# Kernel tuning notes

Measured on AMD Instinct MI355X. Metric: run time of the kernel, lower is better.

## Reference

```python
import jax, jax.numpy as jnp
import numpy as np

D_MODEL = 1024
NHEAD = 16
DFF = 4096
MAXD = 32


def _ln(x, g, b, eps=1e-5):
    mu = jnp.mean(x, axis=-1, keepdims=True)
    var = jnp.mean(jnp.square(x - mu), axis=-1, keepdims=True)
    return (x - mu) * jax.lax.rsqrt(var + eps) * g + b


def setup_inputs() -> dict:
    key = jax.random.key(0)
    ks = jax.random.split(key, 16)
    D, F, H = D_MODEL, DFF, NHEAD
    s = 1.0 / np.sqrt(D)
    inp = {
        "src": jax.random.normal(ks[0], (2, 2048, D), dtype=jnp.float32),
        "Wq": jax.random.normal(ks[1], (D, D), dtype=jnp.float32) * s,
        "Wk": jax.random.normal(ks[2], (D, D), dtype=jnp.float32) * s,
        "Wv": jax.random.normal(ks[3], (D, D), dtype=jnp.float32) * s,
        "bq": jnp.zeros((D,), jnp.float32),
        "bk": jnp.zeros((D,), jnp.float32),
        "bv": jnp.zeros((D,), jnp.float32),
        "Wo": jax.random.normal(ks[4], (D, D), dtype=jnp.float32) * s,
        "bo": jnp.zeros((D,), jnp.float32),
        "rpe_table": jax.random.normal(ks[5], (2 * MAXD + 1, H), dtype=jnp.float32) * 0.02,
        "W1": jax.random.normal(ks[6], (D, F), dtype=jnp.float32) * s,
        "b1": jnp.zeros((F,), jnp.float32),
        "W2": jax.random.normal(ks[7], (F, D), dtype=jnp.float32) * (1.0 / np.sqrt(F)),
        "b2": jnp.zeros((D,), jnp.float32),
        "ln1_g": jnp.ones((D,), jnp.float32),
        "ln1_b": jnp.zeros((D,), jnp.float32),
        "ln2_g": jnp.ones((D,), jnp.float32),
        "ln2_b": jnp.zeros((D,), jnp.float32),
    }
    return inp


def reference(src, Wq, Wk, Wv, bq, bk, bv, Wo, bo, rpe_table, W1, b1, W2, b2,
              ln1_g, ln1_b, ln2_g, ln2_b):
    B, L, D = src.shape
    H = NHEAD
    Dh = D // H
    scale = 1.0 / jnp.sqrt(jnp.asarray(Dh, src.dtype))

    # relative position bias: [L, L, H] -> [H, L, L]
    pos = jnp.arange(L)
    rel = jnp.clip(pos[None, :] - pos[:, None], -MAXD, MAXD) + MAXD  # [L, L]
    bias = jnp.transpose(rpe_table[rel], (2, 0, 1))  # [H, L, L]

    q = (src @ Wq + bq).reshape(B, L, H, Dh)
    k = (src @ Wk + bk).reshape(B, L, H, Dh)
    v = (src @ Wv + bv).reshape(B, L, H, Dh)

    scores = jnp.einsum("blhd,bmhd->bhlm", q, k) * scale + bias[None]
    attn = jax.nn.softmax(scores, axis=-1)
    ctx = jnp.einsum("bhlm,bmhd->blhd", attn, v).reshape(B, L, D)
    attn_out = ctx @ Wo + bo

    x = _ln(src + attn_out, ln1_g, ln1_b)
    ff = jax.nn.relu(x @ W1 + b1) @ W2 + b2
    return _ln(x + ff, ln2_g, ln2_b)
```

## Files before the change

kernel.cpp:

```cpp
#include <hip/hip_runtime.h>
#include <hip/hip_bf16.h>

#define D_MODEL 1024
#define NHEAD 16
#define DH 64
#define DFF 4096
#define MAXD 32
#define L_ 2048
#define NROW 4096

typedef __attribute__((ext_vector_type(4))) float floatx4;
typedef __attribute__((ext_vector_type(8))) __bf16 bf16x8;
typedef __attribute__((ext_vector_type(4))) unsigned short ushort4v;

static __device__ inline unsigned short f2bf(float f) {
    __hip_bfloat16 h = __float2bfloat16(f);
    return __builtin_bit_cast(unsigned short, h);
}

static __device__ inline floatx4 mfma16(bf16x8 a, bf16x8 b, floatx4 c) {
    return __builtin_amdgcn_mfma_f32_16x16x32_bf16(a, b, c, 0, 0, 0);
}

static __device__ inline void gload_lds16(const unsigned short* g, unsigned short* l) {
    __builtin_amdgcn_global_load_lds((const __attribute__((address_space(1))) unsigned int*)g,
                                     (__attribute__((address_space(3))) unsigned int*)l,
                                     16, 0, 0);
}

__global__ __launch_bounds__(256) void cast_bf16_kernel(const float* __restrict__ in,
                                                        unsigned short* __restrict__ out, int n4) {
    int i = blockIdx.x * 256 + threadIdx.x;
    if (i < n4) {
        floatx4 v = *(const floatx4*)&in[(size_t)i * 4];
        ushort4v o;
        o.x = f2bf(v[0]); o.y = f2bf(v[1]); o.z = f2bf(v[2]); o.w = f2bf(v[3]);
        *(ushort4v*)&out[(size_t)i * 4] = o;
    }
}

__global__ __launch_bounds__(256) void transpose_cast_kernel(const float* __restrict__ W,
                                                             unsigned short* __restrict__ WT,
                                                             int K, int N) {
    __shared__ float tile[32][33];
    int k0 = blockIdx.y * 32, n0 = blockIdx.x * 32;
    for (int i = threadIdx.x; i < 1024; i += 256) {
        int r = i >> 5, c = i & 31;
        tile[r][c] = W[(size_t)(k0 + r) * N + n0 + c];
    }
    __syncthreads();
    for (int i = threadIdx.x; i < 1024; i += 256) {
        int r = i >> 5, c = i & 31;
        WT[(size_t)(n0 + r) * K + k0 + c] = f2bf(tile[c][r]);
    }
}

__global__ __launch_bounds__(256) void pack_bias_kernel(const float* __restrict__ bq,
                                                        const float* __restrict__ bk,
                                                        const float* __restrict__ bv,
                                                        float* __restrict__ out) {
    int i = blockIdx.x * 256 + threadIdx.x;
    if (i < 3072) out[i] = (i < 1024) ? bq[i] : ((i < 2048) ? bk[i - 1024] : bv[i - 2048]);
}

template <int NF, bool OUTBF16, bool RELU>
__global__ __launch_bounds__(256) void gemm_kernel(const unsigned short* __restrict__ A,
                                                   const unsigned short* __restrict__ BT,
                                                   const float* __restrict__ bias,
                                                   void* __restrict__ Cout,
                                                   int M, int N, int K) {
    constexpr int BN = NF * 32;
    __shared__ unsigned short Asm[128][32];
    __shared__ unsigned short Bsm[BN][32];
    int t = threadIdx.x;
    int lane = t & 63, w = t >> 6;
    int wm = w >> 1, wn = w & 1;
    int lr = lane & 15, hg = lane >> 4;
    int m0 = blockIdx.y * 128, n0 = blockIdx.x * BN;

    floatx4 acc[4][NF];
#pragma unroll
    for (int i = 0; i < 4; i++)
#pragma unroll
        for (int j = 0; j < NF; j++) acc[i][j] = (floatx4)0.0f;

    int r0 = t >> 2, c0 = (t & 3) * 8;

    for (int k0 = 0; k0 < K; k0 += 32) {
        __syncthreads();
        gload_lds16(&A[(size_t)(m0 + r0) * K + k0 + c0], &Asm[r0][c0]);
        gload_lds16(&A[(size_t)(m0 + r0 + 64) * K + k0 + c0], &Asm[r0 + 64][c0]);
        gload_lds16(&BT[(size_t)(n0 + r0) * K + k0 + c0], &Bsm[r0][c0]);
        if (NF == 4)
            gload_lds16(&BT[(size_t)(n0 + r0 + 64) * K + k0 + c0], &Bsm[r0 + 64][c0]);
        __syncthreads();
        bf16x8 af[4], bfg[NF];
#pragma unroll
        for (int mf = 0; mf < 4; mf++) af[mf] = *(const bf16x8*)&Asm[wm * 64 + mf * 16 + lr][hg * 8];
#pragma unroll
        for (int nf = 0; nf < NF; nf++)
            bfg[nf] = *(const bf16x8*)&Bsm[wn * NF * 16 + nf * 16 + lr][hg * 8];
#pragma unroll
        for (int mf = 0; mf < 4; mf++)
#pragma unroll
            for (int nf = 0; nf < NF; nf++) acc[mf][nf] = mfma16(af[mf], bfg[nf], acc[mf][nf]);
    }

#pragma unroll
    for (int mf = 0; mf < 4; mf++)
#pragma unroll
        for (int nf = 0; nf < NF; nf++) {
            int col = n0 + wn * NF * 16 + nf * 16 + lr;
            float bv = bias[col];
#pragma unroll
            for (int r = 0; r < 4; r++) {
                int row = m0 + wm * 64 + mf * 16 + hg * 4 + r;
                float v = acc[mf][nf][r] + bv;
                if (RELU) v = v > 0.f ? v : 0.f;
                if (OUTBF16)
                    ((unsigned short*)Cout)[(size_t)row * N + col] = f2bf(v);
                else
                    ((float*)Cout)[(size_t)row * N + col] = v;
            }
        }
}

__global__ __launch_bounds__(512, 4) void attn_kernel(const unsigned short* __restrict__ qkv,
                                                      const float* __restrict__ rpe,
                                                      unsigned short* __restrict__ ctx) {
    __shared__ unsigned short Kb0[64 * 64];
    __shared__ unsigned short Kb1[64 * 64];
    __shared__ unsigned short Vt[64 * 64];
    __shared__ unsigned short Ps[8][16 * 64];
    __shared__ float rpl[65];

    const int t = threadIdx.x;
    const int lane = t & 63, w = t >> 6;
    const int lr = lane & 15, hg = lane >> 4;
    const int lrs = (lr & 7) ^ (lr >> 3);

    const int blk = blockIdx.x;
    const int qb = blk & 15;
    const int h = (blk >> 4) & 15;
    const int b = blk >> 8;
    const int q0 = qb * 128;
    const int hcol = h * 64;
    const size_t rowbase = (size_t)b * L_ * 3072;

    const int kr = t >> 3, kch = t & 7;
    const int kswz = (kch ^ (kr & 7) ^ (kr >> 3)) & 7;
    unsigned short* kdst0 = &Kb0[kr * 64 + kch * 8];
    unsigned short* kdst1 = &Kb1[kr * 64 + kch * 8];

    if (t < 65) rpl[t] = rpe[t * NHEAD + h];

    const int qi = q0 + w * 16 + lr;
    bf16x8 qf0 = *(const bf16x8*)&qkv[rowbase + (size_t)qi * 3072 + hcol + hg * 8];
    bf16x8 qf1 = *(const bf16x8*)&qkv[rowbase + (size_t)qi * 3072 + hcol + 32 + hg * 8];

    gload_lds16(&qkv[rowbase + (size_t)kr * 3072 + 1024 + hcol + kswz * 8], kdst0);
    __syncthreads();

    float rpl0 = rpl[0], rpl64 = rpl[64];
    floatx4 o[4];
#pragma unroll
    for (int df = 0; df < 4; df++) o[df] = (floatx4)0.f;
    float mst = -1e30f, lst = 0.f;
    const float scale = 0.125f;
    unsigned short* PsW = &Ps[w][0];

#define ATT_STEP(KT, KcP, KnP, MORE)                                                               \
    {                                                                                              \
        const int key0 = (KT) * 64;                                                                \
        int4 tv = *(const int4*)&qkv[rowbase + (size_t)(key0 + kr) * 3072 + 2048 + hcol + kch * 8];\
        if (MORE)                                                                                  \
            gload_lds16(&qkv[rowbase + (size_t)(key0 + 64 + kr) * 3072 + 1024 + hcol + kswz * 8],  \
                        KnP);                                                                      \
        floatx4 st[4];                                                                             \
        _Pragma("unroll")                                                                          \
        for (int kf = 0; kf < 4; kf++) {                                                           \
            int sw = lrs ^ (kf * 2);                                                               \
            bf16x8 a0 = *(const bf16x8*)&(KcP)[(kf * 16 + lr) * 64 + ((hg ^ sw) << 3)];            \
            bf16x8 a1 = *(const bf16x8*)&(KcP)[(kf * 16 + lr) * 64 + (((4 + hg) ^ sw) << 3)];      \
            st[kf] = mfma16(a1, qf1, mfma16(a0, qf0, (floatx4)0.f));                               \
        }                                                                                          \
        bool rightC = (key0 > q0 + 159);                                                           \
        bool leftC = (key0 + 95 < q0);                                                             \
        float cbv = rightC ? rpl64 : rpl0;                                                         \
        float sv[16];                                                                              \
        float mx = -1e30f;                                                                         \
        if (leftC || rightC) {                                                                     \
            _Pragma("unroll")                                                                      \
            for (int kf = 0; kf < 4; kf++)                                                         \
                _Pragma("unroll")                                                                  \
                for (int r = 0; r < 4; r++) {                                                      \
                    float v = st[kf][r] * scale + cbv;                                             \
                    sv[kf * 4 + r] = v;                                                            \
                    mx = fmaxf(mx, v);                                                             \
                }                                                                                  \
        } else {                                                                                   \
            _Pragma("unroll")                                                                      \
            for (int kf = 0; kf < 4; kf++)                                                         \
                _Pragma("unroll")                                                                  \
                for (int r = 0; r < 4; r++) {                                                      \
                    int rel = key0 + kf * 16 + hg * 4 + r - qi;                                    \
                    rel = rel < -MAXD ? -MAXD : (rel > MAXD ? MAXD : rel);                         \
                    float v = st[kf][r] * scale + rpl[rel + MAXD];                                 \
                    sv[kf * 4 + r] = v;                                                            \
                    mx = fmaxf(mx, v);                                                             \
                }                                                                                  \
        }                                                                                          \
        mx = fmaxf(mx, __shfl_xor(mx, 16, 64));                                                    \
        mx = fmaxf(mx, __shfl_xor(mx, 32, 64));                                                    \
        float newm = fmaxf(mst, mx);                                                               \
        float corr = __expf(mst - newm);                                                           \
        mst = newm;                                                                                \
        float ps = 0.f;                                                                            \
        unsigned int pk[8];                                                                        \
        _Pragma("unroll")                                                                          \
        for (int kf = 0; kf < 4; kf++)                                                             \
            _Pragma("unroll")                                                                      \
            for (int j = 0; j < 2; j++) {                                                          \
                float p0 = __expf(sv[kf * 4 + 2 * j] - newm);                                      \
                float p1 = __expf(sv[kf * 4 + 2 * j + 1] - newm);                                  \
                ps += p0 + p1;                                                                     \
                pk[kf * 2 + j] = (unsigned int)f2bf(p0) | ((unsigned int)f2bf(p1) << 16);          \
            }                                                                                      \
        lst = lst * corr + ps;                                                                     \
        _Pragma("unroll")                                                                          \
        for (int df = 0; df < 4; df++) o[df] *= corr;                                              \
        _Pragma("unroll")                                                                          \
        for (int kf = 0; kf < 4; kf++)                                                             \
            _Pragma("unroll")                                                                      \
            for (int j = 0; j < 2; j++) {                                                          \
                int ch = ((kf * 2 + (hg >> 1)) ^ lrs) & 7;                                         \
                *(unsigned int*)&PsW[lr * 64 + (ch << 3) + (hg & 1) * 4 + 2 * j] = pk[kf * 2 + j]; \
            }                                                                                      \
        _Pragma("unroll")                                                                          \
        for (int e = 0; e < 8; e++) {                                                              \
            int d = kch * 8 + e;                                                                   \
            int ch = ((kr >> 3) ^ e ^ kch) & 7;                                                    \
            unsigned short val = (unsigned short)(((const unsigned int*)&tv)[e >> 1] >>            \
                                                  ((e & 1) * 16));                                 \
            Vt[d * 64 + (ch << 3) + (kr & 7)] = val;                                               \
        }                                                                                          \
        __syncthreads();                                                                           \
        bf16x8 pb0 = *(const bf16x8*)&PsW[lr * 64 + ((hg ^ lrs) << 3)];                            \
        bf16x8 pb1 = *(const bf16x8*)&PsW[lr * 64 + (((4 + hg) ^ lrs) << 3)];                      \
        _Pragma("unroll")                                                                          \
        for (int df = 0; df < 4; df++) {                                                           \
            int sw = lrs ^ (df * 2);                                                               \
            bf16x8 v0 = *(const bf16x8*)&Vt[(df * 16 + lr) * 64 + ((hg ^ sw) << 3)];               \
            bf16x8 v1 = *(const bf16x8*)&Vt[(df * 16 + lr) * 64 + (((4 + hg) ^ sw) << 3)];         \
            o[df] = mfma16(v1, pb1, mfma16(v0, pb0, o[df]));                                       \
        }                                                                                          \
        __syncthreads();                                                                           \
    }

    for (int kt = 0; kt < L_ / 64; kt += 2) {
        ATT_STEP(kt, Kb0, kdst1, true);
        ATT_STEP(kt + 1, Kb1, kdst0, (kt + 2 < L_ / 64));
    }
#undef ATT_STEP

    float rs = lst;
    rs += __shfl_xor(rs, 16, 64);
    rs += __shfl_xor(rs, 32, 64);
    float inv = 1.f / rs;
    size_t obase = (size_t)(b * L_ + qi) * 1024 + hcol;
#pragma unroll
    for (int df = 0; df < 4; df++)
#pragma unroll
        for (int r = 0; r < 4; r++)
            ctx[obase + df * 16 + hg * 4 + r] = f2bf(o[df][r] * inv);
}

template <bool WBF>
__global__ __launch_bounds__(256) void resln_kernel(const float* __restrict__ ra,
                                                    const float* __restrict__ rb,
                                                    const float* __restrict__ g,
                                                    const float* __restrict__ be,
                                                    float* __restrict__ outf,
                                                    unsigned short* __restrict__ outb) {
    __shared__ float red[4];
    __shared__ float red2[4];
    int row = blockIdx.x;
    int t = threadIdx.x;
    int w = t >> 6, lane = t & 63;
    size_t base = (size_t)row * 1024 + t * 4;
    floatx4 a = *(const floatx4*)&ra[base];
    floatx4 b = *(const floatx4*)&rb[base];
    floatx4 y = a + b;
    float s = y[0] + y[1] + y[2] + y[3];
#pragma unroll
    for (int d = 1; d < 64; d <<= 1) s += __shfl_xor(s, d, 64);
    if (lane == 0) red[w] = s;
    __syncthreads();
    float mu = (red[0] + red[1] + red[2] + red[3]) * (1.f / 1024.f);
    floatx4 d4 = y - mu;
    float sq = d4[0] * d4[0] + d4[1] * d4[1] + d4[2] * d4[2] + d4[3] * d4[3];
#pragma unroll
    for (int d = 1; d < 64; d <<= 1) sq += __shfl_xor(sq, d, 64);
    if (lane == 0) red2[w] = sq;
    __syncthreads();
    float var = (red2[0] + red2[1] + red2[2] + red2[3]) * (1.f / 1024.f);
    float rstd = rsqrtf(var + 1e-5f);
    floatx4 gg = *(const floatx4*)&g[t * 4];
    floatx4 bb = *(const floatx4*)&be[t * 4];
    floatx4 outv;
#pragma unroll
    for (int i = 0; i < 4; i++) outv[i] = d4[i] * rstd * gg[i] + bb[i];
    *(floatx4*)&outf[base] = outv;
    if (WBF) {
        ushort4v ov;
        ov.x = f2bf(outv[0]); ov.y = f2bf(outv[1]); ov.z = f2bf(outv[2]); ov.w = f2bf(outv[3]);
        *(ushort4v*)&outb[base] = ov;
    }
}

extern "C" void kernel_launch(void* const* d_in, const int* in_sizes, int n_in,
                              void* d_out, int out_size, void* d_ws, size_t ws_size,
                              hipStream_t stream) {
    const float* src = (const float*)d_in[0];
    const float* Wq = (const float*)d_in[1];
    const float* Wk = (const float*)d_in[2];
    const float* Wv = (const float*)d_in[3];
    const float* bq = (const float*)d_in[4];
    const float* bk = (const float*)d_in[5];
    const float* bv = (const float*)d_in[6];
    const float* Wo = (const float*)d_in[7];
    const float* bo = (const float*)d_in[8];
    const float* rpe = (const float*)d_in[9];
    const float* W1 = (const float*)d_in[10];
    const float* b1 = (const float*)d_in[11];
    const float* W2 = (const float*)d_in[12];
    const float* b2 = (const float*)d_in[13];
    const float* ln1g = (const float*)d_in[14];
    const float* ln1b = (const float*)d_in[15];
    const float* ln2g = (const float*)d_in[16];
    const float* ln2b = (const float*)d_in[17];
    float* out = (float*)d_out;
    char* ws = (char*)d_ws;

    const size_t o_srcb = 0;
    const size_t o_wtqkv = o_srcb + 8388608;
    const size_t o_wto = o_wtqkv + 6291456;
    const size_t o_wt1 = o_wto + 2097152;
    const size_t o_wt2 = o_wt1 + 8388608;
    const size_t o_bqkv = o_wt2 + 8388608;
    const size_t o_qkv = o_bqkv + 12288;
    const size_t o_ctxb = o_qkv + 25165824;
    const size_t o_x = o_ctxb + 8388608;
    const size_t o_hb = o_x + 16777216;

    unsigned short* srcb = (unsigned short*)(ws + o_srcb);
    unsigned short* wtqkv = (unsigned short*)(ws + o_wtqkv);
    unsigned short* wto = (unsigned short*)(ws + o_wto);
    unsigned short* wt1 = (unsigned short*)(ws + o_wt1);
    unsigned short* wt2 = (unsigned short*)(ws + o_wt2);
    float* bqkv = (float*)(ws + o_bqkv);
    unsigned short* qkvb = (unsigned short*)(ws + o_qkv);
    unsigned short* ctxb = (unsigned short*)(ws + o_ctxb);
    float* x = (float*)(ws + o_x);
    unsigned short* hb = (unsigned short*)(ws + o_hb);
    float* attnout = (float*)(ws + o_qkv);
    float* ff = (float*)(ws + o_qkv);
    unsigned short* xb = (unsigned short*)(ws + o_srcb);

    cast_bf16_kernel<<<4096, 256, 0, stream>>>(src, srcb, 1048576);
    transpose_cast_kernel<<<dim3(32, 32), 256, 0, stream>>>(Wq, wtqkv, 1024, 1024);
    transpose_cast_kernel<<<dim3(32, 32), 256, 0, stream>>>(Wk, wtqkv + 1024 * 1024, 1024, 1024);
    transpose_cast_kernel<<<dim3(32, 32), 256, 0, stream>>>(Wv, wtqkv + 2 * 1024 * 1024, 1024, 1024);
    transpose_cast_kernel<<<dim3(32, 32), 256, 0, stream>>>(Wo, wto, 1024, 1024);
    transpose_cast_kernel<<<dim3(128, 32), 256, 0, stream>>>(W1, wt1, 1024, 4096);
    transpose_cast_kernel<<<dim3(32, 128), 256, 0, stream>>>(W2, wt2, 4096, 1024);
    pack_bias_kernel<<<12, 256, 0, stream>>>(bq, bk, bv, bqkv);

    gemm_kernel<4, true, false><<<dim3(24, 32), 256, 0, stream>>>(srcb, wtqkv, bqkv, qkvb, NROW, 3072, 1024);
    attn_kernel<<<512, 512, 0, stream>>>(qkvb, rpe, ctxb);
    gemm_kernel<2, false, false><<<dim3(16, 32), 256, 0, stream>>>(ctxb, wto, bo, attnout, NROW, 1024, 1024);
    resln_kernel<true><<<4096, 256, 0, stream>>>(src, attnout, ln1g, ln1b, x, xb);
    gemm_kernel<4, true, true><<<dim3(32, 32), 256, 0, stream>>>(xb, wt1, b1, hb, NROW, 4096, 1024);
    gemm_kernel<2, false, false><<<dim3(16, 32), 256, 0, stream>>>(hb, wt2, b2, ff, NROW, 1024, 4096);
    resln_kernel<false><<<4096, 256, 0, stream>>>(x, ff, ln2g, ln2b, out, nullptr);
}
```

Measured before the change: 346.3 us.

## Double-buffer GEMM LDS tiles and shrink attention blocks to 64 queries

The GEMM kernel now uses two LDS buffers for A and B. It issues the next K-slice's async loads before computing on the current one, which overlaps global-to-LDS transfer with MFMA work and halves the number of barriers per K element. Separately, the attention kernel moves from 512-thread blocks covering 128 queries to 256-thread blocks covering 64 queries. Each thread now loads two K/V rows, and a block-index remap interleaves blocks across the grid. The attention change doubles the block count for better occupancy and load spread, but it doubles K/V reloads per query and increases LDS use in the GEMM.

```diff
diff --git a/kernel.cpp b/kernel.cpp
--- a/kernel.cpp
+++ b/kernel.cpp
@@ -63,6 +63,22 @@
     if (i < 3072) out[i] = (i < 1024) ? bq[i] : ((i < 2048) ? bk[i - 1024] : bv[i - 2048]);
 }
 
+#define GEMM_COMPUTE(As, Bs)                                                        \
+    {                                                                               \
+        bf16x8 af[4], bfg[NF];                                                      \
+        _Pragma("unroll")                                                           \
+        for (int mf = 0; mf < 4; mf++)                                              \
+            af[mf] = *(const bf16x8*)&As[wm * 64 + mf * 16 + lr][hg * 8];           \
+        _Pragma("unroll")                                                           \
+        for (int nf = 0; nf < NF; nf++)                                             \
+            bfg[nf] = *(const bf16x8*)&Bs[wn * NF * 16 + nf * 16 + lr][hg * 8];     \
+        _Pragma("unroll")                                                           \
+        for (int mf = 0; mf < 4; mf++)                                              \
+            _Pragma("unroll")                                                       \
+            for (int nf = 0; nf < NF; nf++)                                         \
+                acc[mf][nf] = mfma16(af[mf], bfg[nf], acc[mf][nf]);                 \
+    }
+
 template <int NF, bool OUTBF16, bool RELU>
 __global__ __launch_bounds__(256) void gemm_kernel(const unsigned short* __restrict__ A,
                                                    const unsigned short* __restrict__ BT,
@@ -70,8 +86,8 @@
                                                    void* __restrict__ Cout,
                                                    int M, int N, int K) {
     constexpr int BN = NF * 32;
-    __shared__ unsigned short Asm[128][32];
-    __shared__ unsigned short Bsm[BN][32];
+    __shared__ unsigned short A0[128][32], A1[128][32];
+    __shared__ unsigned short B0[BN][32], B1[BN][32];
     int t = threadIdx.x;
     int lane = t & 63, w = t >> 6;
     int wm = w >> 1, wn = w & 1;
@@ -85,25 +101,32 @@
         for (int j = 0; j < NF; j++) acc[i][j] = (floatx4)0.0f;
 
     int r0 = t >> 2, c0 = (t & 3) * 8;
-
-    for (int k0 = 0; k0 < K; k0 += 32) {
+    const unsigned short* Arow0 = &A[(size_t)(m0 + r0) * K + c0];
+    const unsigned short* Arow1 = &A[(size_t)(m0 + r0 + 64) * K + c0];
+    const unsigned short* Brow0 = &BT[(size_t)(n0 + r0) * K + c0];
+    const unsigned short* Brow1 = &BT[(size_t)(n0 + r0 + 64) * K + c0];
+
+    gload_lds16(Arow0, &A0[r0][c0]);
+    gload_lds16(Arow1, &A0[r0 + 64][c0]);
+    gload_lds16(Brow0, &B0[r0][c0]);
+    if (NF == 4) gload_lds16(Brow1, &B0[r0 + 64][c0]);
+    __syncthreads();
+
+    for (int k0 = 0; k0 < K; k0 += 64) {
+        gload_lds16(Arow0 + k0 + 32, &A1[r0][c0]);
+        gload_lds16(Arow1 + k0 + 32, &A1[r0 + 64][c0]);
+        gload_lds16(Brow0 + k0 + 32, &B1[r0][c0]);
+        if (NF == 4) gload_lds16(Brow1 + k0 + 32, &B1[r0 + 64][c0]);
+        GEMM_COMPUTE(A0, B0);
         __syncthreads();
-        gload_lds16(&A[(size_t)(m0 + r0) * K + k0 + c0], &Asm[r0][c0]);
-        gload_lds16(&A[(size_t)(m0 + r0 + 64) * K + k0 + c0], &Asm[r0 + 64][c0]);
-        gload_lds16(&BT[(size_t)(n0 + r0) * K + k0 + c0], &Bsm[r0][c0]);
-        if (NF == 4)
-            gload_lds16(&BT[(size_t)(n0 + r0 + 64) * K + k0 + c0], &Bsm[r0 + 64][c0]);
+        if (k0 + 64 < K) {
+            gload_lds16(Arow0 + k0 + 64, &A0[r0][c0]);
+            gload_lds16(Arow1 + k0 + 64, &A0[r0 + 64][c0]);
+            gload_lds16(Brow0 + k0 + 64, &B0[r0][c0]);
+            if (NF == 4) gload_lds16(Brow1 + k0 + 64, &B0[r0 + 64][c0]);
+        }
+        GEMM_COMPUTE(A1, B1);
         __syncthreads();
-        bf16x8 af[4], bfg[NF];
-#pragma unroll
-        for (int mf = 0; mf < 4; mf++) af[mf] = *(const bf16x8*)&Asm[wm * 64 + mf * 16 + lr][hg * 8];
-#pragma unroll
-        for (int nf = 0; nf < NF; nf++)
-            bfg[nf] = *(const bf16x8*)&Bsm[wn * NF * 16 + nf * 16 + lr][hg * 8];
-#pragma unroll
-        for (int mf = 0; mf < 4; mf++)
-#pragma unroll
-            for (int nf = 0; nf < NF; nf++) acc[mf][nf] = mfma16(af[mf], bfg[nf], acc[mf][nf]);
     }
 
 #pragma unroll
@@ -125,13 +148,13 @@
         }
 }
 
-__global__ __launch_bounds__(512, 4) void attn_kernel(const unsigned short* __restrict__ qkv,
+__global__ __launch_bounds__(256, 4) void attn_kernel(const unsigned short* __restrict__ qkv,
                                                       const float* __restrict__ rpe,
                                                       unsigned short* __restrict__ ctx) {
     __shared__ unsigned short Kb0[64 * 64];
     __shared__ unsigned short Kb1[64 * 64];
     __shared__ unsigned short Vt[64 * 64];
-    __shared__ unsigned short Ps[8][16 * 64];
+    __shared__ unsigned short Ps[4][16 * 64];
     __shared__ float rpl[65];
 
     const int t = threadIdx.x;
@@ -139,18 +162,22 @@
     const int lr = lane & 15, hg = lane >> 4;
     const int lrs = (lr & 7) ^ (lr >> 3);
 
-    const int blk = blockIdx.x;
-    const int qb = blk & 15;
-    const int h = (blk >> 4) & 15;
-    const int b = blk >> 8;
-    const int q0 = qb * 128;
+    const int g = blockIdx.x;
+    const int blk = (g & 7) * 128 + (g >> 3);
+    const int qb = blk & 31;
+    const int h = (blk >> 5) & 15;
+    const int b = blk >> 9;
+    const int q0 = qb * 64;
     const int hcol = h * 64;
     const size_t rowbase = (size_t)b * L_ * 3072;
 
     const int kr = t >> 3, kch = t & 7;
-    const int kswz = (kch ^ (kr & 7) ^ (kr >> 3)) & 7;
-    unsigned short* kdst0 = &Kb0[kr * 64 + kch * 8];
-    unsigned short* kdst1 = &Kb1[kr * 64 + kch * 8];
+    const int kswz0 = (kch ^ (kr & 7) ^ (kr >> 3)) & 7;
+    const int kswz1 = kswz0 ^ 4;
+    unsigned short* kd0a = &Kb0[kr * 64 + kch * 8];
+    unsigned short* kd0b = &Kb0[(kr + 32) * 64 + kch * 8];
+    unsigned short* kd1a = &Kb1[kr * 64 + kch * 8];
+    unsigned short* kd1b = &Kb1[(kr + 32) * 64 + kch * 8];
 
     if (t < 65) rpl[t] = rpe[t * NHEAD + h];
 
@@ -158,7 +185,8 @@
     bf16x8 qf0 = *(const bf16x8*)&qkv[rowbase + (size_t)qi * 3072 + hcol + hg * 8];
     bf16x8 qf1 = *(const bf16x8*)&qkv[rowbase + (size_t)qi * 3072 + hcol + 32 + hg * 8];
 
-    gload_lds16(&qkv[rowbase + (size_t)kr * 3072 + 1024 + hcol + kswz * 8], kdst0);
+    gload_lds16(&qkv[rowbase + (size_t)kr * 3072 + 1024 + hcol + kswz0 * 8], kd0a);
+    gload_lds16(&qkv[rowbase + (size_t)(kr + 32) * 3072 + 1024 + hcol + kswz1 * 8], kd0b);
     __syncthreads();
 
     float rpl0 = rpl[0], rpl64 = rpl[64];
@@ -169,13 +197,18 @@
     const float scale = 0.125f;
     unsigned short* PsW = &Ps[w][0];
 
-#define ATT_STEP(KT, KcP, KnP, MORE)                                                               \
+#define ATT_STEP(KT, KcP, KnA, KnB, MORE)                                                          \
     {                                                                                              \
         const int key0 = (KT) * 64;                                                                \
-        int4 tv = *(const int4*)&qkv[rowbase + (size_t)(key0 + kr) * 3072 + 2048 + hcol + kch * 8];\
-        if (MORE)                                                                                  \
-            gload_lds16(&qkv[rowbase + (size_t)(key0 + 64 + kr) * 3072 + 1024 + hcol + kswz * 8],  \
-                        KnP);                                                                      \
+        int4 tva = *(const int4*)&qkv[rowbase + (size_t)(key0 + kr) * 3072 + 2048 + hcol + kch * 8];\
+        int4 tvb =                                                                                 \
+            *(const int4*)&qkv[rowbase + (size_t)(key0 + kr + 32) * 3072 + 2048 + hcol + kch * 8]; \
+        if (MORE) {                                                                                \
+            gload_lds16(&qkv[rowbase + (size_t)(key0 + 64 + kr) * 3072 + 1024 + hcol + kswz0 * 8], \
+                        KnA);                                                                      \
+            gload_lds16(&qkv[rowbase + (size_t)(key0 + 96 + kr) * 3072 + 1024 + hcol + kswz1 * 8], \
+                        KnB);                                                                      \
+        }                                                                                          \
         floatx4 st[4];                                                                             \
         _Pragma("unroll")                                                                          \
         for (int kf = 0; kf < 4; kf++) {                                                           \
@@ -184,7 +217,7 @@
             bf16x8 a1 = *(const bf16x8*)&(KcP)[(kf * 16 + lr) * 64 + (((4 + hg) ^ sw) << 3)];      \
             st[kf] = mfma16(a1, qf1, mfma16(a0, qf0, (floatx4)0.f));                               \
         }                                                                                          \
-        bool rightC = (key0 > q0 + 159);                                                           \
+        bool rightC = (key0 > q0 + 95);                                                            \
         bool leftC = (key0 + 95 < q0);                                                             \
         float cbv = rightC ? rpl64 : rpl0;                                                         \
         float sv[16];                                                                              \
@@ -239,10 +272,13 @@
         _Pragma("unroll")                                                                          \
         for (int e = 0; e < 8; e++) {                                                              \
             int d = kch * 8 + e;                                                                   \
-            int ch = ((kr >> 3) ^ e ^ kch) & 7;                                                    \
-            unsigned short val = (unsigned short)(((const unsigned int*)&tv)[e >> 1] >>            \
-                                                  ((e & 1) * 16));                                 \
-            Vt[d * 64 + (ch << 3) + (kr & 7)] = val;                                               \
+            int cha = ((kr >> 3) ^ e ^ kch) & 7;                                                   \
+            unsigned short va = (unsigned short)(((const unsigned int*)&tva)[e >> 1] >>            \
+                                                 ((e & 1) * 16));                                  \
+            unsigned short vb = (unsigned short)(((const unsigned int*)&tvb)[e >> 1] >>            \
+                                                 ((e & 1) * 16));                                  \
+            Vt[d * 64 + (cha << 3) + (kr & 7)] = va;                                               \
+            Vt[d * 64 + ((cha ^ 4) << 3) + (kr & 7)] = vb;                                         \
         }                                                                                          \
         __syncthreads();                                                                           \
         bf16x8 pb0 = *(const bf16x8*)&PsW[lr * 64 + ((hg ^ lrs) << 3)];                            \
@@ -258,8 +294,8 @@
     }
 
     for (int kt = 0; kt < L_ / 64; kt += 2) {
-        ATT_STEP(kt, Kb0, kdst1, true);
-        ATT_STEP(kt + 1, Kb1, kdst0, (kt + 2 < L_ / 64));
+        ATT_STEP(kt, Kb0, kd1a, kd1b, true);
+        ATT_STEP(kt + 1, Kb1, kd0a, kd0b, (kt + 2 < L_ / 64));
     }
 #undef ATT_STEP
 
@@ -377,7 +413,7 @@
     pack_bias_kernel<<<12, 256, 0, stream>>>(bq, bk, bv, bqkv);
 
     gemm_kernel<4, true, false><<<dim3(24, 32), 256, 0, stream>>>(srcb, wtqkv, bqkv, qkvb, NROW, 3072, 1024);
-    attn_kernel<<<512, 512, 0, stream>>>(qkvb, rpe, ctxb);
+    attn_kernel<<<1024, 256, 0, stream>>>(qkvb, rpe, ctxb);
     gemm_kernel<2, false, false><<<dim3(16, 32), 256, 0, stream>>>(ctxb, wto, bo, attnout, NROW, 1024, 1024);
     resln_kernel<true><<<4096, 256, 0, stream>>>(src, attnout, ln1g, ln1b, x, xb);
     gemm_kernel<4, true, true><<<dim3(32, 32), 256, 0, stream>>>(xb, wt1, b1, hb, NROW, 4096, 1024);
```

After: 372.0 us. +7.4%, slower.
